# Kernel tuning notes

Hardware: AMD Instinct MI355X
Metric: run time of the kernel (lower is better)

Reference implementation:

```python
import jax, jax.numpy as jnp
import numpy as np

N = 150000
E = 600000
IN_DIM = 128
HID = 64


def setup_inputs() -> dict:
    key = jax.random.key(0)
    ks = jax.random.split(key, 8)
    obs = jax.random.normal(ks[0], (N, IN_DIM), dtype=jnp.float32)
    edge_index = jax.random.randint(ks[1], (2, E), 0, N, dtype=jnp.int64)
    # GCNConv / Linear parameters (PyTorch layout: W is [out, in])
    W1 = jax.random.normal(ks[2], (HID, IN_DIM), dtype=jnp.float32) / np.sqrt(IN_DIM)
    b1 = jnp.zeros((HID,), dtype=jnp.float32)
    W2 = jax.random.normal(ks[3], (HID, HID), dtype=jnp.float32) / np.sqrt(HID)
    b2 = jnp.zeros((HID,), dtype=jnp.float32)
    W3 = jax.random.normal(ks[4], (1, HID), dtype=jnp.float32) / np.sqrt(HID)
    b3 = jnp.zeros((1,), dtype=jnp.float32)
    return {"obs": obs, "edge_index": edge_index, "W1": W1, "b1": b1,
            "W2": W2, "b2": b2, "W3": W3, "b3": b3}


def _gcn_norm(edge_index, n):
    # PyG gcn_norm: add self-loops, symmetric normalization D^-1/2 A D^-1/2
    loops = jnp.arange(n, dtype=edge_index.dtype)
    row = jnp.concatenate([edge_index[0], loops])  # source
    col = jnp.concatenate([edge_index[1], loops])  # target
    deg = jax.ops.segment_sum(jnp.ones(row.shape[0], jnp.float32), col, num_segments=n)
    dinv = jnp.where(deg > 0, jax.lax.rsqrt(deg), 0.0)
    norm = dinv[row] * dinv[col]  # [E+N]
    return row, col, norm


def _gcn_conv(x, row, col, norm, n, W, b):
    # x' = lin(x); out[col] += norm * x'[row]; out += bias
    xw = x @ W.T                     # [N, out]
    msg = xw[row] * norm[:, None]    # gather + scale, [E+N, out]
    out = jax.ops.segment_sum(msg, col, num_segments=n)
    return out + b


def reference(obs, edge_index, W1, b1, W2, b2, W3, b3):
    n = obs.shape[0]
    row, col, norm = _gcn_norm(edge_index, n)
    h1 = jax.nn.relu(_gcn_conv(obs, row, col, norm, n, W1, b1))
    h2 = jax.nn.relu(_gcn_conv(h1, row, col, norm, n, W2, b2))
    out = h2 @ W3.T + b3             # [N, 1]
    out = out.reshape(-1, 15)[:, 3:].reshape(-1)  # drop first 3 of every 15
    return out
```

## Files before the change

kernel.cpp:

```cpp
#include <hip/hip_runtime.h>

#define NN 150000
#define NE 600000
#define IND 128
#define HID 64
#define KMAX 32
#define BSHIFT 8
#define NBUCK 586
#define SUBCAP 224
#define PARTB 293
#define GEMM_GRID ((NN + 63) / 64)
#define NOUT 120000

typedef short s16x8 __attribute__((ext_vector_type(8)));
typedef float f32x4 __attribute__((ext_vector_type(4)));

__device__ __forceinline__ unsigned f2bf(float f) {
    unsigned u = __float_as_uint(f);
    return (u + 0x7FFFu + ((u >> 16) & 1u)) >> 16;
}

#define ACC4(v, dr) \
    a0 = fmaf(__uint_as_float((v).x << 16), dr, a0); \
    a1 = fmaf(__uint_as_float((v).x & 0xFFFF0000u), dr, a1); \
    a2 = fmaf(__uint_as_float((v).y << 16), dr, a2); \
    a3 = fmaf(__uint_as_float((v).y & 0xFFFF0000u), dr, a3);

__global__ void k_zero(int* __restrict__ gcnt) {
    int t = blockIdx.x * 256 + threadIdx.x;
    if (t < NBUCK * 8) gcnt[t] = 0;
}

__global__ __launch_bounds__(256) void k_part(
        const int* __restrict__ rowv, const int* __restrict__ colv,
        int* __restrict__ gcnt, int2* __restrict__ ebuf) {
    __shared__ int hist[NBUCK];
    __shared__ int bases[NBUCK];
    int tid = threadIdx.x;
    for (int i = tid; i < NBUCK; i += 256) hist[i] = 0;
    __syncthreads();
    int4 r4[2], c4[2];
    int bk[8], sl[8];
    bool val[2];
    #pragma unroll
    for (int h = 0; h < 2; ++h) {
        int t = blockIdx.x * 512 + h * 256 + tid;
        val[h] = (t < NE / 4);
        if (val[h]) {
            r4[h] = ((const int4*)rowv)[t];
            c4[h] = ((const int4*)colv)[t];
            bk[4*h+0] = c4[h].x >> BSHIFT; sl[4*h+0] = atomicAdd(&hist[bk[4*h+0]], 1);
            bk[4*h+1] = c4[h].y >> BSHIFT; sl[4*h+1] = atomicAdd(&hist[bk[4*h+1]], 1);
            bk[4*h+2] = c4[h].z >> BSHIFT; sl[4*h+2] = atomicAdd(&hist[bk[4*h+2]], 1);
            bk[4*h+3] = c4[h].w >> BSHIFT; sl[4*h+3] = atomicAdd(&hist[bk[4*h+3]], 1);
        }
    }
    __syncthreads();
    int xcd = blockIdx.x & 7;
    for (int i = tid; i < NBUCK; i += 256)
        bases[i] = hist[i] ? atomicAdd(&gcnt[i * 8 + xcd], hist[i]) : 0;
    __syncthreads();
    #pragma unroll
    for (int h = 0; h < 2; ++h) {
        if (val[h]) {
            #pragma unroll
            for (int e = 0; e < 4; ++e) {
                int c = (e == 0) ? c4[h].x : (e == 1) ? c4[h].y : (e == 2) ? c4[h].z : c4[h].w;
                int r = (e == 0) ? r4[h].x : (e == 1) ? r4[h].y : (e == 2) ? r4[h].z : r4[h].w;
                int p = bases[bk[4*h+e]] + sl[4*h+e];
                if (p < SUBCAP) ebuf[(bk[4*h+e] * 8 + xcd) * SUBCAP + p] = make_int2(c, r);
            }
        }
    }
}

__global__ __launch_bounds__(256) void k_sort_gemm1(
        const float* __restrict__ obs, const float* __restrict__ W1,
        unsigned short* __restrict__ xs,
        const int* __restrict__ gcnt, const int2* __restrict__ ebuf,
        int* __restrict__ cursor, float* __restrict__ dinvf,
        int* __restrict__ csr_src) {
    __shared__ char smem[64 * IND * 2];
    int tid = threadIdx.x;
    if (blockIdx.x < NBUCK) {
        int k = blockIdx.x;
        int lo = k << BSHIFT;
        int* cnt = (int*)smem;
        cnt[tid] = 0;
        __syncthreads();
        for (int x = 0; x < 8; ++x) {
            int len = gcnt[k * 8 + x]; if (len > SUBCAP) len = SUBCAP;
            const int2* run = ebuf + (size_t)(k * 8 + x) * SUBCAP;
            for (int i = tid; i < len; i += 256) {
                int2 e = run[i];
                int s = atomicAdd(&cnt[e.x - lo], 1);
                if (s < KMAX) csr_src[e.x * KMAX + s] = e.y;
            }
        }
        __syncthreads();
        int n = lo + tid;
        if (n < NN) {
            cursor[n] = cnt[tid];
            dinvf[n] = rsqrtf((float)(cnt[tid] + 1));
        }
        return;
    }
    char* sB = smem;
    int base = (blockIdx.x - NBUCK) * 64;

    {
        const float4* Wsrc = (const float4*)W1;
        for (int idx = tid; idx < 64 * 32; idx += 256) {
            int row = idx >> 5, c4i = idx & 31;
            float4 w = Wsrc[idx];
            uint2 p;
            p.x = f2bf(w.x) | (f2bf(w.y) << 16);
            p.y = f2bf(w.z) | (f2bf(w.w) << 16);
            int byte = row * (IND * 2) + c4i * 8;
            byte ^= (row & 7) << 4;
            *(uint2*)(sB + byte) = p;
        }
    }
    __syncthreads();

    int wave = tid >> 6, lane = tid & 63;
    int r16 = lane & 15, kg = lane >> 4;
    int arow = base + 16 * wave + r16;
    if (arow >= NN) arow = NN - 1;
    const float4* Ap = (const float4*)(obs + (size_t)arow * IND) + kg * 2;

    float4 va[8];
    #pragma unroll
    for (int s = 0; s < 4; ++s) {
        va[2 * s]     = Ap[s * 8];
        va[2 * s + 1] = Ap[s * 8 + 1];
    }

    f32x4 acc[4];
    #pragma unroll
    for (int j = 0; j < 4; ++j) acc[j] = (f32x4){0.f, 0.f, 0.f, 0.f};

    #pragma unroll
    for (int s = 0; s < 4; ++s) {
        float4 v0 = va[2 * s], v1 = va[2 * s + 1];
        s16x8 a;
        a[0] = (short)f2bf(v0.x); a[1] = (short)f2bf(v0.y);
        a[2] = (short)f2bf(v0.z); a[3] = (short)f2bf(v0.w);
        a[4] = (short)f2bf(v1.x); a[5] = (short)f2bf(v1.y);
        a[6] = (short)f2bf(v1.z); a[7] = (short)f2bf(v1.w);
        int kb = (s * 32 + kg * 8) * 2;
        #pragma unroll
        for (int j = 0; j < 4; ++j) {
            int row = 16 * j + r16;
            int byte = row * (IND * 2) + kb;
            byte ^= (row & 7) << 4;
            s16x8 b = *(const s16x8*)(sB + byte);
            acc[j] = __builtin_amdgcn_mfma_f32_16x16x32_bf16(a, b, acc[j], 0, 0, 0);
        }
    }

    #pragma unroll
    for (int r = 0; r < 4; ++r) {
        int n = base + 16 * wave + kg * 4 + r;
        if (n >= NN) continue;
        #pragma unroll
        for (int j = 0; j < 4; ++j) {
            int c = 16 * j + r16;
            xs[(size_t)n * HID + c] = (unsigned short)f2bf(acc[j][r]);
        }
    }
}

__global__ __launch_bounds__(256) void k_agg_gemm(
        const unsigned short* __restrict__ xs, const int* __restrict__ cursor,
        const float* __restrict__ dinvf, const int* __restrict__ csr_src,
        const float* __restrict__ bias, const float* __restrict__ W2,
        unsigned short* __restrict__ xs2) {
    __shared__ char smem[2 * 64 * HID * 2];
    char* sA = smem;
    char* sB = smem + 64 * HID * 2;
    int tid = threadIdx.x;
    int base = blockIdx.x * 64;

    {
        const float4* Wsrc = (const float4*)W2;
        for (int idx = tid; idx < 64 * 16; idx += 256) {
            int row = idx >> 4, c4i = idx & 15;
            float4 w = Wsrc[idx];
            uint2 p;
            p.x = f2bf(w.x) | (f2bf(w.y) << 16);
            p.y = f2bf(w.z) | (f2bf(w.w) << 16);
            int byte = row * (HID * 2) + c4i * 8;
            byte ^= (row & 7) << 4;
            *(uint2*)(sB + byte) = p;
        }
    }

    int lane = tid & 63;
    int l16 = lane & 15, gbase = lane & 48;
    int grp = tid >> 4;
    const uint2* src = (const uint2*)xs;
    float4 bb = ((const float4*)bias)[l16];

    int degA[4], cntA[4], idxA[4];
    uint2 svA[4];
    float drA[4];
    #pragma unroll
    for (int s4 = 0; s4 < 4; ++s4) {
        int node = base + s4 * 16 + grp;
        bool ok = node < NN;
        int nc = ok ? node : NN - 1;
        int deg = cursor[nc];
        degA[s4] = deg;
        cntA[s4] = ok ? (deg < KMAX ? deg : KMAX) : 0;
        idxA[s4] = csr_src[nc * KMAX + l16];
        svA[s4]  = src[(size_t)nc * 16 + l16];
    }
    #pragma unroll
    for (int s4 = 0; s4 < 4; ++s4) {
        drA[s4] = (l16 < cntA[s4]) ? dinvf[idxA[s4]] : 0.0f;
    }

    #pragma unroll
    for (int s4 = 0; s4 < 4; ++s4) {
        int row = s4 * 16 + grp;
        int node = base + row;
        int cnt = cntA[s4];
        float dn = rsqrtf((float)(degA[s4] + 1));
        uint2 sv = svA[s4];
        float a0 = __uint_as_float(sv.x << 16) * dn;
        float a1 = __uint_as_float(sv.x & 0xFFFF0000u) * dn;
        float a2 = __uint_as_float(sv.y << 16) * dn;
        float a3 = __uint_as_float(sv.y & 0xFFFF0000u) * dn;
        uint2 v[8];
        #pragma unroll
        for (int j = 0; j < 8; ++j) {
            int r = __shfl(idxA[s4], gbase + j, 64);
            r = (j < cnt) ? r : 0;
            v[j] = src[(size_t)r * 16 + l16];
        }
        #pragma unroll
        for (int j = 0; j < 8; ++j) {
            float dr = __shfl(drA[s4], gbase + j, 64);
            ACC4(v[j], dr)
        }
        if (cnt > 8) {
            int c16 = cnt < 16 ? cnt : 16;
            for (int j = 8; j < c16; ++j) {
                int r    = __shfl(idxA[s4], gbase + j, 64);
                float dr = __shfl(drA[s4], gbase + j, 64);
                uint2 vv = src[(size_t)r * 16 + l16];
                ACC4(vv, dr)
            }
            for (int j = 16; j < cnt; ++j) {
                int r = csr_src[node * KMAX + j];
                float dr = dinvf[r];
                uint2 vv = src[(size_t)r * 16 + l16];
                ACC4(vv, dr)
            }
        }
        float h0 = fmaxf(fmaf(dn, a0, bb.x), 0.f);
        float h1 = fmaxf(fmaf(dn, a1, bb.y), 0.f);
        float h2 = fmaxf(fmaf(dn, a2, bb.z), 0.f);
        float h3 = fmaxf(fmaf(dn, a3, bb.w), 0.f);
        uint2 o;
        o.x = f2bf(h0) | (f2bf(h1) << 16);
        o.y = f2bf(h2) | (f2bf(h3) << 16);
        if (node >= NN) { o.x = 0u; o.y = 0u; }
        int byte = row * (HID * 2) + l16 * 8;
        byte ^= (row & 7) << 4;
        *(uint2*)(sA + byte) = o;
    }
    __syncthreads();

    int wave = tid >> 6;
    int wr = wave >> 1, wc = wave & 1;
    int r16 = lane & 15, kg = lane >> 4;

    f32x4 acc[2][2];
    #pragma unroll
    for (int i = 0; i < 2; ++i)
        #pragma unroll
        for (int j = 0; j < 2; ++j)
            acc[i][j] = (f32x4){0.f, 0.f, 0.f, 0.f};

    #pragma unroll
    for (int s = 0; s < HID / 32; ++s) {
        int kb = (s * 32 + kg * 8) * 2;
        s16x8 a[2], b[2];
        #pragma unroll
        for (int i = 0; i < 2; ++i) {
            int row = 32 * wr + 16 * i + r16;
            int byte = row * (HID * 2) + kb;
            byte ^= (row & 7) << 4;
            a[i] = *(const s16x8*)(sA + byte);
        }
        #pragma unroll
        for (int j = 0; j < 2; ++j) {
            int row = 32 * wc + 16 * j + r16;
            int byte = row * (HID * 2) + kb;
            byte ^= (row & 7) << 4;
            b[j] = *(const s16x8*)(sB + byte);
        }
        #pragma unroll
        for (int i = 0; i < 2; ++i)
            #pragma unroll
            for (int j = 0; j < 2; ++j)
                acc[i][j] = __builtin_amdgcn_mfma_f32_16x16x32_bf16(a[i], b[j], acc[i][j], 0, 0, 0);
    }

    #pragma unroll
    for (int i = 0; i < 2; ++i) {
        #pragma unroll
        for (int r = 0; r < 4; ++r) {
            int n = base + 32 * wr + 16 * i + kg * 4 + r;
            if (n >= NN) continue;
            float d = dinvf[n];
            #pragma unroll
            for (int j = 0; j < 2; ++j) {
                int c = 32 * wc + 16 * j + r16;
                xs2[(size_t)n * HID + c] = (unsigned short)f2bf(acc[i][j][r] * d);
            }
        }
    }
}

__global__ __launch_bounds__(256) void k_agg_out(const unsigned short* __restrict__ xs,
                      const int* __restrict__ cursor, const int* __restrict__ csr_src,
                      const float* __restrict__ bias, const float* __restrict__ W3,
                      const float* __restrict__ b3, float* __restrict__ outp) {
    int tid = threadIdx.x;
    int lane = tid & 63;
    int l16 = lane & 15, gbase = lane & 48;
    int q = blockIdx.x * 16 + (tid >> 4);
    if (q >= NOUT) return;
    int g15 = q / 12, jj12 = q - g15 * 12;
    int node = g15 * 15 + 3 + jj12;
    int deg = cursor[node];
    int cnt = deg < KMAX ? deg : KMAX;
    float dn = rsqrtf((float)(deg + 1));
    const uint2* src = (const uint2*)xs;
    int idx0 = csr_src[node * KMAX + l16];
    float w0 = (l16 < cnt) ? 1.0f : 0.0f;
    uint2 sv = src[(size_t)node * 16 + l16];
    float a0 = __uint_as_float(sv.x << 16);
    float a1 = __uint_as_float(sv.x & 0xFFFF0000u);
    float a2 = __uint_as_float(sv.y << 16);
    float a3 = __uint_as_float(sv.y & 0xFFFF0000u);
    uint2 v[8];
    #pragma unroll
    for (int j = 0; j < 8; ++j) {
        int r = __shfl(idx0, gbase + j, 64);
        r = (j < cnt) ? r : 0;
        v[j] = src[(size_t)r * 16 + l16];
    }
    #pragma unroll
    for (int j = 0; j < 8; ++j) {
        float w = __shfl(w0, gbase + j, 64);
        ACC4(v[j], w)
    }
    if (cnt > 8) {
        int c16 = cnt < 16 ? cnt : 16;
        for (int j = 8; j < c16; ++j) {
            int r = __shfl(idx0, gbase + j, 64);
            uint2 vv = src[(size_t)r * 16 + l16];
            ACC4(vv, 1.0f)
        }
        for (int j = 16; j < cnt; ++j) {
            int r = csr_src[node * KMAX + j];
            uint2 vv = src[(size_t)r * 16 + l16];
            ACC4(vv, 1.0f)
        }
    }
    float4 bb = ((const float4*)bias)[l16];
    float h0 = fmaxf(fmaf(dn, a0, bb.x), 0.f);
    float h1 = fmaxf(fmaf(dn, a1, bb.y), 0.f);
    float h2 = fmaxf(fmaf(dn, a2, bb.z), 0.f);
    float h3 = fmaxf(fmaf(dn, a3, bb.w), 0.f);
    float4 ww = ((const float4*)W3)[l16];
    float v3 = h0 * ww.x + h1 * ww.y + h2 * ww.z + h3 * ww.w;
    v3 += __shfl_xor(v3, 1, 64);
    v3 += __shfl_xor(v3, 2, 64);
    v3 += __shfl_xor(v3, 4, 64);
    v3 += __shfl_xor(v3, 8, 64);
    if (l16 == 0) outp[q] = v3 + b3[0];
}

extern "C" void kernel_launch(void* const* d_in, const int* in_sizes, int n_in,
                              void* d_out, int out_size, void* d_ws, size_t ws_size,
                              hipStream_t stream) {
    const float* obs = (const float*)d_in[0];
    const int*   ei  = (const int*)d_in[1];
    const float* W1  = (const float*)d_in[2];
    const float* b1  = (const float*)d_in[3];
    const float* W2  = (const float*)d_in[4];
    const float* b2  = (const float*)d_in[5];
    const float* W3  = (const float*)d_in[6];
    const float* b3  = (const float*)d_in[7];
    float* out = (float*)d_out;

    char* ws = (char*)d_ws;
    size_t off = 0;
    auto alloc = [&](size_t bytes) -> void* {
        void* p = ws + off;
        off += (bytes + 255) & ~(size_t)255;
        return p;
    };
    int*   gcnt    = (int*)  alloc((size_t)NBUCK * 8 * 4);
    int*   cursor  = (int*)  alloc((size_t)NN * 4);
    float* dinvf   = (float*)alloc((size_t)NN * 4);
    int*   csr_src = (int*)  alloc((size_t)NN * KMAX * 4);
    int2*  ebuf    = (int2*) alloc((size_t)NBUCK * 8 * SUBCAP * 8);
    unsigned short* XB  = (unsigned short*)alloc((size_t)NN * HID * 2);
    unsigned short* XB2 = (unsigned short*)alloc((size_t)NN * HID * 2);

    const int* rowv = ei;
    const int* colv = ei + NE;

    k_zero<<<(NBUCK * 8 + 255) / 256, 256, 0, stream>>>(gcnt);
    k_part<<<PARTB, 256, 0, stream>>>(rowv, colv, gcnt, ebuf);
    k_sort_gemm1<<<NBUCK + GEMM_GRID, 256, 0, stream>>>(obs, W1, XB, gcnt, ebuf,
                                                        cursor, dinvf, csr_src);
    k_agg_gemm<<<GEMM_GRID, 256, 0, stream>>>(XB, cursor, dinvf, csr_src, b1, W2, XB2);
    k_agg_out<<<(NOUT + 15) / 16, 256, 0, stream>>>(XB2, cursor, csr_src, b2, W3, b3, out);
}
```

Baseline: 95.53 us.

## Stage CSR buckets in LDS and make GEMM1 blocks loop over tiles with prefetch

The sort blocks now cover 128 nodes each, with twice as many buckets and a smaller sub-capacity. Each block builds its CSR slots in shared memory and writes them out as coalesced int4 stores instead of scattering directly to global memory. The GEMM1 part of the fused kernel now processes four 64-row tiles per block, reusing the bf16 W1 tile in LDS and prefetching the next tile's obs rows into registers. The risks are higher register use, the SUBCAP of 128 possibly dropping edges if a bucket overflows, and k_part having to match the new bucket layout. The full-slot copy also writes uninitialized slots, which should be harmless because only the first cursor entries are read.

```diff
diff --git a/kernel.cpp b/kernel.cpp
--- a/kernel.cpp
+++ b/kernel.cpp
@@ -5,11 +5,12 @@
 #define IND 128
 #define HID 64
 #define KMAX 32
-#define BSHIFT 8
-#define NBUCK 586
-#define SUBCAP 224
+#define BSHIFT 7
+#define NBUCK 1172
+#define SUBCAP 128
 #define PARTB 293
-#define GEMM_GRID ((NN + 63) / 64)
+#define TPB 4
+#define GEMM_BLK 586
 #define NOUT 120000
 
 typedef short s16x8 __attribute__((ext_vector_type(8)));
@@ -80,33 +81,41 @@
         const int* __restrict__ gcnt, const int2* __restrict__ ebuf,
         int* __restrict__ cursor, float* __restrict__ dinvf,
         int* __restrict__ csr_src) {
-    __shared__ char smem[64 * IND * 2];
+    __shared__ int smem_i[128 * KMAX + 128];
     int tid = threadIdx.x;
     if (blockIdx.x < NBUCK) {
         int k = blockIdx.x;
         int lo = k << BSHIFT;
-        int* cnt = (int*)smem;
-        cnt[tid] = 0;
+        int* slots = smem_i;
+        int* cnt   = smem_i + 128 * KMAX;
+        if (tid < 128) cnt[tid] = 0;
         __syncthreads();
         for (int x = 0; x < 8; ++x) {
             int len = gcnt[k * 8 + x]; if (len > SUBCAP) len = SUBCAP;
             const int2* run = ebuf + (size_t)(k * 8 + x) * SUBCAP;
             for (int i = tid; i < len; i += 256) {
                 int2 e = run[i];
-                int s = atomicAdd(&cnt[e.x - lo], 1);
-                if (s < KMAX) csr_src[e.x * KMAX + s] = e.y;
+                int li = e.x - lo;
+                int s = atomicAdd(&cnt[li], 1);
+                if (s < KMAX) slots[li * KMAX + s] = e.y;
             }
         }
         __syncthreads();
-        int n = lo + tid;
-        if (n < NN) {
-            cursor[n] = cnt[tid];
-            dinvf[n] = rsqrtf((float)(cnt[tid] + 1));
+        int4* dst = (int4*)(csr_src + (size_t)lo * KMAX);
+        const int4* s4p = (const int4*)slots;
+        #pragma unroll
+        for (int i = 0; i < 4; ++i) dst[i * 256 + tid] = s4p[i * 256 + tid];
+        if (tid < 128) {
+            int n = lo + tid;
+            if (n < NN) {
+                cursor[n] = cnt[tid];
+                dinvf[n] = rsqrtf((float)(cnt[tid] + 1));
+            }
         }
         return;
     }
-    char* sB = smem;
-    int base = (blockIdx.x - NBUCK) * 64;
+    char* sB = (char*)smem_i;
+    int gblk = blockIdx.x - NBUCK;
 
     {
         const float4* Wsrc = (const float4*)W1;
@@ -125,49 +134,63 @@
 
     int wave = tid >> 6, lane = tid & 63;
     int r16 = lane & 15, kg = lane >> 4;
-    int arow = base + 16 * wave + r16;
-    if (arow >= NN) arow = NN - 1;
-    const float4* Ap = (const float4*)(obs + (size_t)arow * IND) + kg * 2;
-
-    float4 va[8];
-    #pragma unroll
-    for (int s = 0; s < 4; ++s) {
-        va[2 * s]     = Ap[s * 8];
-        va[2 * s + 1] = Ap[s * 8 + 1];
-    }
-
-    f32x4 acc[4];
-    #pragma unroll
-    for (int j = 0; j < 4; ++j) acc[j] = (f32x4){0.f, 0.f, 0.f, 0.f};
-
-    #pragma unroll
-    for (int s = 0; s < 4; ++s) {
-        float4 v0 = va[2 * s], v1 = va[2 * s + 1];
-        s16x8 a;
-        a[0] = (short)f2bf(v0.x); a[1] = (short)f2bf(v0.y);
-        a[2] = (short)f2bf(v0.z); a[3] = (short)f2bf(v0.w);
-        a[4] = (short)f2bf(v1.x); a[5] = (short)f2bf(v1.y);
-        a[6] = (short)f2bf(v1.z); a[7] = (short)f2bf(v1.w);
-        int kb = (s * 32 + kg * 8) * 2;
-        #pragma unroll
-        for (int j = 0; j < 4; ++j) {
-            int row = 16 * j + r16;
-            int byte = row * (IND * 2) + kb;
-            byte ^= (row & 7) << 4;
-            s16x8 b = *(const s16x8*)(sB + byte);
-            acc[j] = __builtin_amdgcn_mfma_f32_16x16x32_bf16(a, b, acc[j], 0, 0, 0);
-        }
-    }
-
-    #pragma unroll
-    for (int r = 0; r < 4; ++r) {
-        int n = base + 16 * wave + kg * 4 + r;
-        if (n >= NN) continue;
-        #pragma unroll
-        for (int j = 0; j < 4; ++j) {
-            int c = 16 * j + r16;
-            xs[(size_t)n * HID + c] = (unsigned short)f2bf(acc[j][r]);
-        }
+
+    float4 vc[8], vn[8];
+    {
+        int arow = gblk * (TPB * 64) + 16 * wave + r16;
+        if (arow >= NN) arow = NN - 1;
+        const float4* Ap = (const float4*)(obs + (size_t)arow * IND) + kg * 2;
+        #pragma unroll
+        for (int s = 0; s < 4; ++s) { vc[2*s] = Ap[s*8]; vc[2*s+1] = Ap[s*8+1]; }
+    }
+
+    #pragma unroll
+    for (int t = 0; t < TPB; ++t) {
+        int base = (gblk * TPB + t) * 64;
+        if (t + 1 < TPB) {
+            int arow = base + 64 + 16 * wave + r16;
+            if (arow >= NN) arow = NN - 1;
+            const float4* Ap = (const float4*)(obs + (size_t)arow * IND) + kg * 2;
+            #pragma unroll
+            for (int s = 0; s < 4; ++s) { vn[2*s] = Ap[s*8]; vn[2*s+1] = Ap[s*8+1]; }
+        }
+
+        f32x4 acc[4];
+        #pragma unroll
+        for (int j = 0; j < 4; ++j) acc[j] = (f32x4){0.f, 0.f, 0.f, 0.f};
+
+        #pragma unroll
+        for (int s = 0; s < 4; ++s) {
+            float4 v0 = vc[2*s], v1 = vc[2*s+1];
+            s16x8 a;
+            a[0] = (short)f2bf(v0.x); a[1] = (short)f2bf(v0.y);
+            a[2] = (short)f2bf(v0.z); a[3] = (short)f2bf(v0.w);
+            a[4] = (short)f2bf(v1.x); a[5] = (short)f2bf(v1.y);
+            a[6] = (short)f2bf(v1.z); a[7] = (short)f2bf(v1.w);
+            int kb = (s * 32 + kg * 8) * 2;
+            #pragma unroll
+            for (int j = 0; j < 4; ++j) {
+                int row = 16 * j + r16;
+                int byte = row * (IND * 2) + kb;
+                byte ^= (row & 7) << 4;
+                s16x8 b = *(const s16x8*)(sB + byte);
+                acc[j] = __builtin_amdgcn_mfma_f32_16x16x32_bf16(a, b, acc[j], 0, 0, 0);
+            }
+        }
+
+        #pragma unroll
+        for (int r = 0; r < 4; ++r) {
+            int n = base + 16 * wave + kg * 4 + r;
+            if (n >= NN) continue;
+            #pragma unroll
+            for (int j = 0; j < 4; ++j) {
+                int c = 16 * j + r16;
+                xs[(size_t)n * HID + c] = (unsigned short)f2bf(acc[j][r]);
+            }
+        }
+
+        #pragma unroll
+        for (int i = 0; i < 8; ++i) vc[i] = vn[i];
     }
 }
 
@@ -419,8 +442,8 @@
 
     k_zero<<<(NBUCK * 8 + 255) / 256, 256, 0, stream>>>(gcnt);
     k_part<<<PARTB, 256, 0, stream>>>(rowv, colv, gcnt, ebuf);
-    k_sort_gemm1<<<NBUCK + GEMM_GRID, 256, 0, stream>>>(obs, W1, XB, gcnt, ebuf,
-                                                        cursor, dinvf, csr_src);
-    k_agg_gemm<<<GEMM_GRID, 256, 0, stream>>>(XB, cursor, dinvf, csr_src, b1, W2, XB2);
+    k_sort_gemm1<<<NBUCK + GEMM_BLK, 256, 0, stream>>>(obs, W1, XB, gcnt, ebuf,
+                                                       cursor, dinvf, csr_src);
+    k_agg_gemm<<<(NN + 63) / 64, 256, 0, stream>>>(XB, cursor, dinvf, csr_src, b1, W2, XB2);
     k_agg_out<<<(NOUT + 15) / 16, 256, 0, stream>>>(XB2, cursor, csr_src, b2, W3, b3, out);
 }
```

Result: slower. 105.2 us (+10.2%).

## Stage GEMM A tiles and outputs through LDS for coalesced loads and stores

Applied to the files above, without the earlier changes.

The first GEMM now converts the obs tile to bf16 into shared memory with coalesced loads and uses a 2x2 wave tiling, like the second GEMM. Both GEMM kernels write results into an LDS tile and then emit 16-byte coalesced stores instead of scattered 2-byte stores. The bucket kernel also loads its eight segment lengths before the barrier. This doubles shared memory in the sort/GEMM kernel and adds barriers, which may reduce occupancy.

```diff
diff --git a/kernel.cpp b/kernel.cpp
--- a/kernel.cpp
+++ b/kernel.cpp
@@ -80,18 +80,23 @@
         const int* __restrict__ gcnt, const int2* __restrict__ ebuf,
         int* __restrict__ cursor, float* __restrict__ dinvf,
         int* __restrict__ csr_src) {
-    __shared__ char smem[64 * IND * 2];
+    __shared__ char smem[2 * 64 * IND * 2];
     int tid = threadIdx.x;
     if (blockIdx.x < NBUCK) {
         int k = blockIdx.x;
         int lo = k << BSHIFT;
         int* cnt = (int*)smem;
         cnt[tid] = 0;
+        int lens[8];
+        #pragma unroll
+        for (int x = 0; x < 8; ++x) {
+            int l = gcnt[k * 8 + x];
+            lens[x] = l > SUBCAP ? SUBCAP : l;
+        }
         __syncthreads();
         for (int x = 0; x < 8; ++x) {
-            int len = gcnt[k * 8 + x]; if (len > SUBCAP) len = SUBCAP;
             const int2* run = ebuf + (size_t)(k * 8 + x) * SUBCAP;
-            for (int i = tid; i < len; i += 256) {
+            for (int i = tid; i < lens[x]; i += 256) {
                 int2 e = run[i];
                 int s = atomicAdd(&cnt[e.x - lo], 1);
                 if (s < KMAX) csr_src[e.x * KMAX + s] = e.y;
@@ -105,7 +110,8 @@
         }
         return;
     }
-    char* sB = smem;
+    char* sA = smem;
+    char* sW = smem + 64 * IND * 2;
     int base = (blockIdx.x - NBUCK) * 64;
 
     {
@@ -118,55 +124,83 @@
             p.y = f2bf(w.z) | (f2bf(w.w) << 16);
             int byte = row * (IND * 2) + c4i * 8;
             byte ^= (row & 7) << 4;
-            *(uint2*)(sB + byte) = p;
+            *(uint2*)(sW + byte) = p;
+        }
+    }
+    {
+        const float4* Xsrc = (const float4*)obs;
+        for (int idx = tid; idx < 64 * 32; idx += 256) {
+            int row = idx >> 5, c4i = idx & 31;
+            int n = base + row; if (n >= NN) n = NN - 1;
+            float4 v = Xsrc[(size_t)n * 32 + c4i];
+            uint2 p;
+            p.x = f2bf(v.x) | (f2bf(v.y) << 16);
+            p.y = f2bf(v.z) | (f2bf(v.w) << 16);
+            int byte = row * (IND * 2) + c4i * 8;
+            byte ^= (row & 7) << 4;
+            *(uint2*)(sA + byte) = p;
         }
     }
     __syncthreads();
 
     int wave = tid >> 6, lane = tid & 63;
+    int wr = wave >> 1, wc = wave & 1;
     int r16 = lane & 15, kg = lane >> 4;
-    int arow = base + 16 * wave + r16;
-    if (arow >= NN) arow = NN - 1;
-    const float4* Ap = (const float4*)(obs + (size_t)arow * IND) + kg * 2;
-
-    float4 va[8];
-    #pragma unroll
-    for (int s = 0; s < 4; ++s) {
-        va[2 * s]     = Ap[s * 8];
-        va[2 * s + 1] = Ap[s * 8 + 1];
-    }
-
-    f32x4 acc[4];
-    #pragma unroll
-    for (int j = 0; j < 4; ++j) acc[j] = (f32x4){0.f, 0.f, 0.f, 0.f};
-
-    #pragma unroll
-    for (int s = 0; s < 4; ++s) {
-        float4 v0 = va[2 * s], v1 = va[2 * s + 1];
-        s16x8 a;
-        a[0] = (short)f2bf(v0.x); a[1] = (short)f2bf(v0.y);
-        a[2] = (short)f2bf(v0.z); a[3] = (short)f2bf(v0.w);
-        a[4] = (short)f2bf(v1.x); a[5] = (short)f2bf(v1.y);
-        a[6] = (short)f2bf(v1.z); a[7] = (short)f2bf(v1.w);
+
+    f32x4 acc[2][2];
+    #pragma unroll
+    for (int i = 0; i < 2; ++i)
+        #pragma unroll
+        for (int j = 0; j < 2; ++j)
+            acc[i][j] = (f32x4){0.f, 0.f, 0.f, 0.f};
+
+    #pragma unroll
+    for (int s = 0; s < IND / 32; ++s) {
         int kb = (s * 32 + kg * 8) * 2;
-        #pragma unroll
-        for (int j = 0; j < 4; ++j) {
-            int row = 16 * j + r16;
+        s16x8 a[2], b[2];
+        #pragma unroll
+        for (int i = 0; i < 2; ++i) {
+            int row = 32 * wr + 16 * i + r16;
             int byte = row * (IND * 2) + kb;
             byte ^= (row & 7) << 4;
-            s16x8 b = *(const s16x8*)(sB + byte);
-            acc[j] = __builtin_amdgcn_mfma_f32_16x16x32_bf16(a, b, acc[j], 0, 0, 0);
-        }
-    }
-
-    #pragma unroll
-    for (int r = 0; r < 4; ++r) {
-        int n = base + 16 * wave + kg * 4 + r;
-        if (n >= NN) continue;
-        #pragma unroll
-        for (int j = 0; j < 4; ++j) {
-            int c = 16 * j + r16;
-            xs[(size_t)n * HID + c] = (unsigned short)f2bf(acc[j][r]);
+            a[i] = *(const s16x8*)(sA + byte);
+        }
+        #pragma unroll
+        for (int j = 0; j < 2; ++j) {
+            int row = 32 * wc + 16 * j + r16;
+            int byte = row * (IND * 2) + kb;
+            byte ^= (row & 7) << 4;
+            b[j] = *(const s16x8*)(sW + byte);
+        }
+        #pragma unroll
+        for (int i = 0; i < 2; ++i)
+            #pragma unroll
+            for (int j = 0; j < 2; ++j)
+                acc[i][j] = __builtin_amdgcn_mfma_f32_16x16x32_bf16(a[i], b[j], acc[i][j], 0, 0, 0);
+    }
+
+    __syncthreads();
+    unsigned short* sC = (unsigned short*)sA;
+    #pragma unroll
+    for (int i = 0; i < 2; ++i) {
+        #pragma unroll
+        for (int r = 0; r < 4; ++r) {
+            int nloc = 32 * wr + 16 * i + kg * 4 + r;
+            #pragma unroll
+            for (int j = 0; j < 2; ++j) {
+                int c = 32 * wc + 16 * j + r16;
+                sC[nloc * 64 + c] = (unsigned short)f2bf(acc[i][j][r]);
+            }
+        }
+    }
+    __syncthreads();
+    {
+        uint4* dst = (uint4*)(xs + (size_t)base * HID);
+        const uint4* s4p = (const uint4*)sC;
+        #pragma unroll
+        for (int k2 = 0; k2 < 2; ++k2) {
+            int idx = k2 * 256 + tid;
+            if (base + (idx >> 3) < NN) dst[idx] = s4p[idx];
         }
     }
 }
@@ -287,7 +321,7 @@
     #pragma unroll
     for (int s = 0; s < HID / 32; ++s) {
         int kb = (s * 32 + kg * 8) * 2;
-        s16x8 a[2], b[2];
+        s16x8 a[2], bfr[2];
         #pragma unroll
         for (int i = 0; i < 2; ++i) {
             int row = 32 * wr + 16 * i + r16;
@@ -300,27 +334,39 @@
             int row = 32 * wc + 16 * j + r16;
             int byte = row * (HID * 2) + kb;
             byte ^= (row & 7) << 4;
-            b[j] = *(const s16x8*)(sB + byte);
+            bfr[j] = *(const s16x8*)(sB + byte);
         }
         #pragma unroll
         for (int i = 0; i < 2; ++i)
             #pragma unroll
             for (int j = 0; j < 2; ++j)
-                acc[i][j] = __builtin_amdgcn_mfma_f32_16x16x32_bf16(a[i], b[j], acc[i][j], 0, 0, 0);
-    }
-
+                acc[i][j] = __builtin_amdgcn_mfma_f32_16x16x32_bf16(a[i], bfr[j], acc[i][j], 0, 0, 0);
+    }
+
+    __syncthreads();
+    unsigned short* sC = (unsigned short*)sA;
     #pragma unroll
     for (int i = 0; i < 2; ++i) {
         #pragma unroll
         for (int r = 0; r < 4; ++r) {
-            int n = base + 32 * wr + 16 * i + kg * 4 + r;
-            if (n >= NN) continue;
-            float d = dinvf[n];
+            int nloc = 32 * wr + 16 * i + kg * 4 + r;
+            int n = base + nloc;
+            float d = dinvf[n < NN ? n : NN - 1];
             #pragma unroll
             for (int j = 0; j < 2; ++j) {
                 int c = 32 * wc + 16 * j + r16;
-                xs2[(size_t)n * HID + c] = (unsigned short)f2bf(acc[i][j][r] * d);
-            }
+                sC[nloc * 64 + c] = (unsigned short)f2bf(acc[i][j][r] * d);
+            }
+        }
+    }
+    __syncthreads();
+    {
+        uint4* dst = (uint4*)(xs2 + (size_t)base * HID);
+        const uint4* s4p = (const uint4*)sC;
+        #pragma unroll
+        for (int k2 = 0; k2 < 2; ++k2) {
+            int idx = k2 * 256 + tid;
+            if (base + (idx >> 3) < NN) dst[idx] = s4p[idx];
         }
     }
 }
```

New measurement: 93.36 us. -2.3%, faster.
